# Kernel tuning notes

Hardware: AMD Instinct MI355X
Metric: run time of the kernel (lower is better)

## Reference

```python
import math
import jax, jax.numpy as jnp
import numpy as np

S, B, H = 512, 64, 1024

def setup_inputs() -> dict:
    key = jax.random.key(0)
    ks = jax.random.split(key, 7)
    hidden = jax.random.normal(ks[0], (1, B, H), dtype=jnp.float32)
    encoder_outputs = jax.random.normal(ks[1], (S, B, H), dtype=jnp.float32)
    pe = jax.random.normal(ks[2], (B, S), dtype=jnp.float32)
    seq_mask = jax.random.bernoulli(ks[3], 0.1, (B, S))
    # nn.Linear(2H, H): weight (H, 2H), bias (H); nn.Linear(H, 1, bias=False): weight (1, H)
    Wa = jax.random.normal(ks[4], (H, 2 * H), dtype=jnp.float32) * (1.0 / math.sqrt(2 * H))
    ba = jax.random.normal(ks[5], (H,), dtype=jnp.float32) * 0.01
    Ws = jax.random.normal(ks[6], (1, H), dtype=jnp.float32) * (1.0 / math.sqrt(H))
    return {"hidden": hidden, "encoder_outputs": encoder_outputs, "pe": pe,
            "seq_mask": seq_mask, "Wa": Wa, "ba": ba, "Ws": Ws}

def reference(hidden, encoder_outputs, pe, seq_mask, Wa, ba, Ws):
    max_len, bsz, hdim = encoder_outputs.shape
    factor = 1.0 / math.sqrt(hdim)
    scale = factor * math.log(max_len)
    # repeat hidden along seq dim, concat on feature dim -> (S, B, 2H)
    h_rep = jnp.broadcast_to(hidden, (max_len, bsz, hdim))
    energy_in = jnp.concatenate([h_rep, encoder_outputs], axis=2)  # (S, B, 2H)
    e = jax.nn.relu(jnp.einsum('sbf,hf->sbh', energy_in, Wa) + ba)  # (S, B, H)
    attn = scale * jnp.einsum('sbh,oh->sbo', e, Ws)[..., 0]          # (S, B)
    attn = attn.T + pe                                               # (B, S)
    attn = jnp.where(seq_mask, jnp.float32(-1e12), attn)
    attn = jax.nn.softmax(attn, axis=1)
    return attn[:, None, :]  # (B, 1, S)
```

## Files before the change

kernel.cpp:

```cpp
#include <hip/hip_runtime.h>
#include <hip/hip_bf16.h>

#define S_LEN 512
#define BSZ 64
#define HDIM 1024
#define H2 2048

typedef float f32x4 __attribute__((ext_vector_type(4)));
typedef short short8 __attribute__((ext_vector_type(8)));
typedef __bf16 bf16x8 __attribute__((ext_vector_type(8)));

__device__ __forceinline__ unsigned short f2bf(float x) {
    union { float f; unsigned u; } v; v.f = x;
    unsigned r = (v.u + 0x7FFFu + ((v.u >> 16) & 1u)) >> 16;
    return (unsigned short)r;
}

__global__ __launch_bounds__(256) void k_zero(float* __restrict__ p) {
    p[blockIdx.x * 256 + threadIdx.x] = 0.f;
}

__global__ __launch_bounds__(256) void k_e1(const float* __restrict__ hidden,
                                            const float* __restrict__ Wa,
                                            const float* __restrict__ ba,
                                            float* __restrict__ e1) {
    __shared__ __align__(16) float hsh[HDIM];
    int b = blockIdx.x >> 2;
    int h = ((blockIdx.x & 3) << 8) + threadIdx.x;
    for (int i = threadIdx.x; i < HDIM; i += 256) hsh[i] = hidden[b * HDIM + i];
    __syncthreads();
    const float* wr = Wa + (size_t)h * H2;
    float acc = 0.f;
#pragma unroll 8
    for (int k = 0; k < HDIM; k += 4) {
        f32x4 w = *(const f32x4*)(wr + k);
        f32x4 hh = *(const f32x4*)(hsh + k);
        acc += w[0] * hh[0] + w[1] * hh[1] + w[2] * hh[2] + w[3] * hh[3];
    }
    e1[b * HDIM + h] = acc + ba[h];
}

__global__ __launch_bounds__(256) void k_packB(const float* __restrict__ Wa,
                                               unsigned short* __restrict__ wsB) {
    int ci = blockIdx.x * 256 + threadIdx.x;
    int tile = ci >> 9;
    int wi = ci & 511;
    int row = wi >> 2;
    int slot = wi & 3;
    int nt = tile >> 5, kt = tile & 31;
    int n = nt * 128 + row;
    int kk = kt * 32 + ((slot ^ ((row >> 1) & 3)) << 3);
    const float* src = Wa + (size_t)n * H2 + HDIM + kk;
    f32x4 a = *(const f32x4*)src;
    f32x4 b = *(const f32x4*)(src + 4);
    short8 o;
    o[0] = (short)f2bf(a[0]); o[1] = (short)f2bf(a[1]);
    o[2] = (short)f2bf(a[2]); o[3] = (short)f2bf(a[3]);
    o[4] = (short)f2bf(b[0]); o[5] = (short)f2bf(b[1]);
    o[6] = (short)f2bf(b[2]); o[7] = (short)f2bf(b[3]);
    *(short8*)(wsB + (size_t)ci * 8) = o;
}

__global__ __launch_bounds__(256) void k_main(const float* __restrict__ enc,
                                              const unsigned short* __restrict__ wsB,
                                              const float* __restrict__ e1,
                                              const float* __restrict__ Ws,
                                              float* __restrict__ logits) {
    __shared__ __align__(16) unsigned short As[4096];
    __shared__ __align__(16) unsigned short Bs[4096];

    int i = blockIdx.x;
    int mt = ((i >> 6) << 3) | (i & 7);
    int nt = (i >> 3) & 7;
    int r0 = mt * 128;
    int n0 = nt * 128;

    int tid = threadIdx.x;
    int lane = tid & 63, wid = tid >> 6;
    int wr = wid >> 1, wc = wid & 1;
    int c = lane & 15, g = lane >> 4;

    f32x4 acc[4][4] = {};

    for (int k0 = 0; k0 < HDIM; k0 += 32) {
        const unsigned short* bsrc = wsB + ((size_t)(nt * 32 + (k0 >> 5)) << 12);
        char* lbase = (char*)Bs + wid * 1024;
        __builtin_amdgcn_global_load_lds(
            (const __attribute__((address_space(1))) void*)(bsrc + (size_t)tid * 8),
            (__attribute__((address_space(3))) void*)lbase, 16, 0, 0);
        __builtin_amdgcn_global_load_lds(
            (const __attribute__((address_space(1))) void*)(bsrc + (size_t)(tid + 256) * 8),
            (__attribute__((address_space(3))) void*)(lbase + 4096), 16, 0, 0);

#pragma unroll
        for (int it = 0; it < 2; ++it) {
            int row = (it << 6) + (tid >> 2);
            int slot = tid & 3;
            int kk = k0 + ((slot ^ ((row >> 1) & 3)) << 3);
            const float* src = enc + (size_t)(r0 + row) * HDIM + kk;
            f32x4 a = *(const f32x4*)src;
            f32x4 b = *(const f32x4*)(src + 4);
            short8 o;
            o[0] = (short)f2bf(a[0]); o[1] = (short)f2bf(a[1]);
            o[2] = (short)f2bf(a[2]); o[3] = (short)f2bf(a[3]);
            o[4] = (short)f2bf(b[0]); o[5] = (short)f2bf(b[1]);
            o[6] = (short)f2bf(b[2]); o[7] = (short)f2bf(b[3]);
            *(short8*)((char*)As + row * 64 + slot * 16) = o;
        }
        __syncthreads();

        bf16x8 af[4], bfr[4];
#pragma unroll
        for (int m = 0; m < 4; ++m) {
            int row = wr * 64 + m * 16 + c;
            int slot = g ^ ((row >> 1) & 3);
            af[m] = *(const bf16x8*)((const char*)As + row * 64 + slot * 16);
        }
#pragma unroll
        for (int n = 0; n < 4; ++n) {
            int rowb = wc * 64 + n * 16 + c;
            int slot = g ^ ((rowb >> 1) & 3);
            bfr[n] = *(const bf16x8*)((const char*)Bs + rowb * 64 + slot * 16);
        }
#pragma unroll
        for (int m = 0; m < 4; ++m)
#pragma unroll
            for (int n = 0; n < 4; ++n)
                acc[m][n] = __builtin_amdgcn_mfma_f32_16x16x32_bf16(af[m], bfr[n], acc[m][n], 0, 0, 0);
        __syncthreads();
    }

    float wsv[4];
#pragma unroll
    for (int n = 0; n < 4; ++n) wsv[n] = Ws[n0 + wc * 64 + n * 16 + c];

#pragma unroll
    for (int m = 0; m < 4; ++m) {
#pragma unroll
        for (int j = 0; j < 4; ++j) {
            int rl = wr * 64 + m * 16 + g * 4 + j;
            int r = r0 + rl;
            int b = r & 63, sidx = r >> 6;
            const float* e1b = e1 + b * HDIM + n0 + wc * 64;
            float p = 0.f;
#pragma unroll
            for (int n = 0; n < 4; ++n) {
                float v = acc[m][n][j] + e1b[n * 16 + c];
                v = fmaxf(v, 0.f);
                p += v * wsv[n];
            }
            p += __shfl_xor(p, 1);
            p += __shfl_xor(p, 2);
            p += __shfl_xor(p, 4);
            p += __shfl_xor(p, 8);
            if (c == 0) atomicAdd(&logits[b * S_LEN + sidx], p);
        }
    }
}

__global__ __launch_bounds__(512) void k_softmax(float* __restrict__ out,
                                                 const float* __restrict__ pe,
                                                 const int* __restrict__ mask,
                                                 float scale) {
    __shared__ float red[8];
    int b = blockIdx.x, s = threadIdx.x;
    int idx = (b << 9) + s;
    float acc = out[idx];
    float logit = (mask[idx] != 0) ? -1e12f : (scale * acc + pe[idx]);
    float m = logit;
#pragma unroll
    for (int o = 32; o >= 1; o >>= 1) m = fmaxf(m, __shfl_xor(m, o));
    if ((s & 63) == 0) red[s >> 6] = m;
    __syncthreads();
    float m2 = red[0];
#pragma unroll
    for (int i2 = 1; i2 < 8; ++i2) m2 = fmaxf(m2, red[i2]);
    float e = expf(logit - m2);
    float t = e;
#pragma unroll
    for (int o = 32; o >= 1; o >>= 1) t += __shfl_xor(t, o);
    __syncthreads();
    if ((s & 63) == 0) red[s >> 6] = t;
    __syncthreads();
    float tot = 0.f;
#pragma unroll
    for (int i2 = 0; i2 < 8; ++i2) tot += red[i2];
    out[idx] = e / tot;
}

extern "C" void kernel_launch(void* const* d_in, const int* in_sizes, int n_in,
                              void* d_out, int out_size, void* d_ws, size_t ws_size,
                              hipStream_t stream) {
    const float* hidden = (const float*)d_in[0];
    const float* enc    = (const float*)d_in[1];
    const float* pe     = (const float*)d_in[2];
    const int*   mask   = (const int*)d_in[3];
    const float* Wa     = (const float*)d_in[4];
    const float* ba     = (const float*)d_in[5];
    const float* Ws     = (const float*)d_in[6];
    float* out = (float*)d_out;

    float* e1 = (float*)d_ws;
    unsigned short* wsB = (unsigned short*)((char*)d_ws + 262144);

    const float scale = 0.19494764453248462f;

    k_zero<<<128, 256, 0, stream>>>(out);
    k_e1<<<256, 256, 0, stream>>>(hidden, Wa, ba, e1);
    k_packB<<<512, 256, 0, stream>>>(Wa, wsB);
    k_main<<<2048, 256, 0, stream>>>(enc, wsB, e1, Ws, out);
    k_softmax<<<64, 512, 0, stream>>>(out, pe, mask, scale);
}
```

Measured before the change: 393.3 us.

## Prefetch encoder tiles in registers, restructure e1 GEMV, fold zeroing into packB

The main GEMM loop now register-prefetches the next K-slice of fp32 encoder data while converting the current one to bf16. It uses explicit waitcnt and raw barriers so the global loads overlap the LDS stores and MFMA work. k_e1 is reorganised so each wavefront computes one output column for all 64 batches, reading each Wa row once instead of 64 times, with hidden staged in padded shared memory. The separate zeroing kernel is merged into k_packB, and the manual bf16 rounding is replaced by native __bf16 casts. The hand-written waitcnt and barrier scheduling carries ordering risk if the compiler's load counts differ from what it assumes.

```diff
diff --git a/kernel.cpp b/kernel.cpp
--- a/kernel.cpp
+++ b/kernel.cpp
@@ -2,47 +2,52 @@
 #include <hip/hip_bf16.h>
 
 #define S_LEN 512
-#define BSZ 64
 #define HDIM 1024
 #define H2 2048
 
 typedef float f32x4 __attribute__((ext_vector_type(4)));
-typedef short short8 __attribute__((ext_vector_type(8)));
+typedef float f32x2 __attribute__((ext_vector_type(2)));
 typedef __bf16 bf16x8 __attribute__((ext_vector_type(8)));
 
-__device__ __forceinline__ unsigned short f2bf(float x) {
-    union { float f; unsigned u; } v; v.f = x;
-    unsigned r = (v.u + 0x7FFFu + ((v.u >> 16) & 1u)) >> 16;
-    return (unsigned short)r;
-}
-
-__global__ __launch_bounds__(256) void k_zero(float* __restrict__ p) {
-    p[blockIdx.x * 256 + threadIdx.x] = 0.f;
-}
-
+#define E1_PITCH 258
 __global__ __launch_bounds__(256) void k_e1(const float* __restrict__ hidden,
                                             const float* __restrict__ Wa,
                                             const float* __restrict__ ba,
                                             float* __restrict__ e1) {
-    __shared__ __align__(16) float hsh[HDIM];
-    int b = blockIdx.x >> 2;
-    int h = ((blockIdx.x & 3) << 8) + threadIdx.x;
-    for (int i = threadIdx.x; i < HDIM; i += 256) hsh[i] = hidden[b * HDIM + i];
-    __syncthreads();
-    const float* wr = Wa + (size_t)h * H2;
+    __shared__ float hsh[64 * E1_PITCH];
+    int h = blockIdx.x * 4 + (threadIdx.x >> 6);
+    int lane = threadIdx.x & 63;
+    const float* wrow = Wa + (size_t)h * H2;
     float acc = 0.f;
+    for (int k0 = 0; k0 < HDIM; k0 += 256) {
+        __syncthreads();
+        for (int idx = threadIdx.x; idx < 4096; idx += 256) {
+            int b = idx >> 6, ck = (idx & 63) << 2;
+            f32x4 v = *(const f32x4*)(hidden + b * HDIM + k0 + ck);
+            f32x2 lo; lo[0] = v[0]; lo[1] = v[1];
+            f32x2 hi; hi[0] = v[2]; hi[1] = v[3];
+            *(f32x2*)(hsh + b * E1_PITCH + ck) = lo;
+            *(f32x2*)(hsh + b * E1_PITCH + ck + 2) = hi;
+        }
+        __syncthreads();
+        const float* wr = wrow + k0;
+        const float* hb = hsh + lane * E1_PITCH;
 #pragma unroll 8
-    for (int k = 0; k < HDIM; k += 4) {
-        f32x4 w = *(const f32x4*)(wr + k);
-        f32x4 hh = *(const f32x4*)(hsh + k);
-        acc += w[0] * hh[0] + w[1] * hh[1] + w[2] * hh[2] + w[3] * hh[3];
+        for (int kk = 0; kk < 256; kk += 4) {
+            f32x4 w = *(const f32x4*)(wr + kk);
+            f32x2 h01 = *(const f32x2*)(hb + kk);
+            f32x2 h23 = *(const f32x2*)(hb + kk + 2);
+            acc += w[0] * h01[0] + w[1] * h01[1] + w[2] * h23[0] + w[3] * h23[1];
+        }
     }
-    e1[b * HDIM + h] = acc + ba[h];
+    e1[lane * HDIM + h] = acc + ba[h];
 }
 
 __global__ __launch_bounds__(256) void k_packB(const float* __restrict__ Wa,
-                                               unsigned short* __restrict__ wsB) {
+                                               unsigned short* __restrict__ wsB,
+                                               float* __restrict__ logits) {
     int ci = blockIdx.x * 256 + threadIdx.x;
+    if (ci < S_LEN * 64) logits[ci] = 0.f;
     int tile = ci >> 9;
     int wi = ci & 511;
     int row = wi >> 2;
@@ -53,12 +58,10 @@
     const float* src = Wa + (size_t)n * H2 + HDIM + kk;
     f32x4 a = *(const f32x4*)src;
     f32x4 b = *(const f32x4*)(src + 4);
-    short8 o;
-    o[0] = (short)f2bf(a[0]); o[1] = (short)f2bf(a[1]);
-    o[2] = (short)f2bf(a[2]); o[3] = (short)f2bf(a[3]);
-    o[4] = (short)f2bf(b[0]); o[5] = (short)f2bf(b[1]);
-    o[6] = (short)f2bf(b[2]); o[7] = (short)f2bf(b[3]);
-    *(short8*)(wsB + (size_t)ci * 8) = o;
+    bf16x8 o;
+    o[0] = (__bf16)a[0]; o[1] = (__bf16)a[1]; o[2] = (__bf16)a[2]; o[3] = (__bf16)a[3];
+    o[4] = (__bf16)b[0]; o[5] = (__bf16)b[1]; o[6] = (__bf16)b[2]; o[7] = (__bf16)b[3];
+    *(bf16x8*)(wsB + (size_t)ci * 8) = o;
 }
 
 __global__ __launch_bounds__(256) void k_main(const float* __restrict__ enc,
@@ -80,34 +83,48 @@
     int wr = wid >> 1, wc = wid & 1;
     int c = lane & 15, g = lane >> 4;
 
+    int rowA = tid >> 2;
+    int slotA = tid & 3;
+    int kkA = (slotA ^ ((rowA >> 1) & 3)) << 3;
+    const float* aptr0 = enc + (size_t)(r0 + rowA) * HDIM + kkA;
+    const float* aptr1 = aptr0 + (size_t)64 * HDIM;
+
     f32x4 acc[4][4] = {};
 
-    for (int k0 = 0; k0 < HDIM; k0 += 32) {
-        const unsigned short* bsrc = wsB + ((size_t)(nt * 32 + (k0 >> 5)) << 12);
-        char* lbase = (char*)Bs + wid * 1024;
+    f32x4 c0 = *(const f32x4*)(aptr0);
+    f32x4 c1 = *(const f32x4*)(aptr0 + 4);
+    f32x4 c2 = *(const f32x4*)(aptr1);
+    f32x4 c3 = *(const f32x4*)(aptr1 + 4);
+
+    for (int kt = 0; kt < 32; ++kt) {
+        const unsigned short* bsrc = wsB + ((size_t)(nt * 32 + kt) << 12);
+        char* lb = (char*)Bs + wid * 1024;
         __builtin_amdgcn_global_load_lds(
             (const __attribute__((address_space(1))) void*)(bsrc + (size_t)tid * 8),
-            (__attribute__((address_space(3))) void*)lbase, 16, 0, 0);
+            (__attribute__((address_space(3))) void*)lb, 16, 0, 0);
         __builtin_amdgcn_global_load_lds(
             (const __attribute__((address_space(1))) void*)(bsrc + (size_t)(tid + 256) * 8),
-            (__attribute__((address_space(3))) void*)(lbase + 4096), 16, 0, 0);
-
-#pragma unroll
-        for (int it = 0; it < 2; ++it) {
-            int row = (it << 6) + (tid >> 2);
-            int slot = tid & 3;
-            int kk = k0 + ((slot ^ ((row >> 1) & 3)) << 3);
-            const float* src = enc + (size_t)(r0 + row) * HDIM + kk;
-            f32x4 a = *(const f32x4*)src;
-            f32x4 b = *(const f32x4*)(src + 4);
-            short8 o;
-            o[0] = (short)f2bf(a[0]); o[1] = (short)f2bf(a[1]);
-            o[2] = (short)f2bf(a[2]); o[3] = (short)f2bf(a[3]);
-            o[4] = (short)f2bf(b[0]); o[5] = (short)f2bf(b[1]);
-            o[6] = (short)f2bf(b[2]); o[7] = (short)f2bf(b[3]);
-            *(short8*)((char*)As + row * 64 + slot * 16) = o;
-        }
-        __syncthreads();
+            (__attribute__((address_space(3))) void*)(lb + 4096), 16, 0, 0);
+        __builtin_amdgcn_sched_barrier(0);
+
+        int kn = (kt < 31) ? kt + 1 : 31;
+        f32x4 n0v = *(const f32x4*)(aptr0 + kn * 32);
+        f32x4 n1v = *(const f32x4*)(aptr0 + kn * 32 + 4);
+        f32x4 n2v = *(const f32x4*)(aptr1 + kn * 32);
+        f32x4 n3v = *(const f32x4*)(aptr1 + kn * 32 + 4);
+
+        bf16x8 o0, o1;
+        o0[0] = (__bf16)c0[0]; o0[1] = (__bf16)c0[1]; o0[2] = (__bf16)c0[2]; o0[3] = (__bf16)c0[3];
+        o0[4] = (__bf16)c1[0]; o0[5] = (__bf16)c1[1]; o0[6] = (__bf16)c1[2]; o0[7] = (__bf16)c1[3];
+        o1[0] = (__bf16)c2[0]; o1[1] = (__bf16)c2[1]; o1[2] = (__bf16)c2[2]; o1[3] = (__bf16)c2[3];
+        o1[4] = (__bf16)c3[0]; o1[5] = (__bf16)c3[1]; o1[6] = (__bf16)c3[2]; o1[7] = (__bf16)c3[3];
+        *(bf16x8*)((char*)As + (rowA << 6) + (slotA << 4)) = o0;
+        *(bf16x8*)((char*)As + ((rowA + 64) << 6) + (slotA << 4)) = o1;
+
+        asm volatile("s_waitcnt vmcnt(4) lgkmcnt(0)" ::: "memory");
+        __builtin_amdgcn_sched_barrier(0);
+        __builtin_amdgcn_s_barrier();
+        __builtin_amdgcn_sched_barrier(0);
 
         bf16x8 af[4], bfr[4];
 #pragma unroll
@@ -127,7 +144,12 @@
 #pragma unroll
             for (int n = 0; n < 4; ++n)
                 acc[m][n] = __builtin_amdgcn_mfma_f32_16x16x32_bf16(af[m], bfr[n], acc[m][n], 0, 0, 0);
-        __syncthreads();
+
+        __builtin_amdgcn_sched_barrier(0);
+        __builtin_amdgcn_s_barrier();
+        __builtin_amdgcn_sched_barrier(0);
+
+        c0 = n0v; c1 = n1v; c2 = n2v; c3 = n3v;
     }
 
     float wsv[4];
@@ -205,9 +227,8 @@
 
     const float scale = 0.19494764453248462f;
 
-    k_zero<<<128, 256, 0, stream>>>(out);
     k_e1<<<256, 256, 0, stream>>>(hidden, Wa, ba, e1);
-    k_packB<<<512, 256, 0, stream>>>(Wa, wsB);
+    k_packB<<<512, 256, 0, stream>>>(Wa, wsB, out);
     k_main<<<2048, 256, 0, stream>>>(enc, wsB, e1, Ws, out);
     k_softmax<<<64, 512, 0, stream>>>(out, pe, mask, scale);
 }
```

New measurement: 398.4 us. No clear change (+1.3%).
